# Kernel optimization log

Measured on AMD Instinct MI355X. Metric: run time of the kernel, lower is better.

The kernel has to match this reference:

```python
import jax, jax.numpy as jnp
import numpy as np


def _conv(x, w, b, stride):
    y = jax.lax.conv_general_dilated(x, w, (stride, stride), [(1, 1), (1, 1)],
                                     dimension_numbers=('NCHW', 'OIHW', 'NCHW'))
    return y + b[None, :, None, None]


def _prelu(x, a):
    return jnp.where(x >= 0, x, a[None, :, None, None] * x)


def _conv2_block(x, wa, ba, aa, wb, bb, ab):
    # conv2 = stride-2 conv + PReLU, then stride-1 conv + PReLU (RIFE-style)
    x = _prelu(_conv(x, wa, ba, 2), aa)
    return _prelu(_conv(x, wb, bb, 1), ab)


def _halve_flow(flow):
    # F.interpolate(scale_factor=0.5, bilinear, align_corners=False) on exact
    # half-downsampling == 2x2 average pooling; then * 0.5 rescales flow units.
    B, C, H, W = flow.shape
    return flow.reshape(B, C, H // 2, 2, W // 2, 2).mean(axis=(3, 5)) * 0.5


def _splat_one(inp, flow):
    # inp [C,H,W], flow [2,H,W]: bilinear forward-splat (scatter-add) summation
    C, H, W = inp.shape
    gx = jnp.arange(W, dtype=flow.dtype)
    gy = jnp.arange(H, dtype=flow.dtype)
    fx = flow[0] + gx[None, :]  # target x coord per source pixel
    fy = flow[1] + gy[:, None]
    x0 = jnp.floor(fx); y0 = jnp.floor(fy)
    x1 = x0 + 1.0;      y1 = y0 + 1.0
    src = inp.reshape(C, H * W)
    out = jnp.zeros((C, H * W), inp.dtype)
    corners = [(x0, y0, (x1 - fx) * (y1 - fy)),
               (x1, y0, (fx - x0) * (y1 - fy)),
               (x0, y1, (x1 - fx) * (fy - y0)),
               (x1, y1, (fx - x0) * (fy - y0))]
    for xi, yi, w in corners:
        valid = (xi >= 0) & (xi < W) & (yi >= 0) & (yi < H)
        idx = yi.astype(jnp.int32) * W + xi.astype(jnp.int32)
        idx = jnp.where(valid, idx, 0).reshape(-1)
        wv = jnp.where(valid, w, 0.0).reshape(-1)
        out = out.at[:, idx].add(src * wv[None, :])
    return out.reshape(C, H, W)


def _softsplat_avg(inp, flow):
    # strType='average': splat features and a ones channel, divide by count
    num = jax.vmap(_splat_one)(inp, flow)
    cnt = jax.vmap(_splat_one)(jnp.ones_like(inp[:, :1]), flow)
    return num / jnp.where(cnt == 0.0, 1.0, cnt)


def setup_inputs() -> dict:
    key = jax.random.key(0)
    ks = jax.random.split(key, 12)
    B, H, W = 16, 512, 512
    d = {
        'img': jax.random.normal(ks[0], (B, 3, H, W), jnp.float32),
        'flow': jax.random.normal(ks[1], (B, 2, H, W), jnp.float32) * 4.0,
    }
    c = 16
    chans = [(3, c), (c, 2 * c), (2 * c, 4 * c), (4 * c, 8 * c)]
    for i, (ci, co) in enumerate(chans, start=1):
        ka, kb = jax.random.split(ks[1 + i], 2)
        d[f'w{i}a'] = jax.random.normal(ka, (co, ci, 3, 3), jnp.float32) * 0.1
        d[f'b{i}a'] = jnp.zeros((co,), jnp.float32)
        d[f'a{i}a'] = jnp.full((co,), 0.25, jnp.float32)
        d[f'w{i}b'] = jax.random.normal(kb, (co, co, 3, 3), jnp.float32) * 0.1
        d[f'b{i}b'] = jnp.zeros((co,), jnp.float32)
        d[f'a{i}b'] = jnp.full((co,), 0.25, jnp.float32)
    return d


def reference(img, flow,
              w1a, b1a, a1a, w1b, b1b, a1b,
              w2a, b2a, a2a, w2b, b2b, a2b,
              w3a, b3a, a3a, w3b, b3b, a3b,
              w4a, b4a, a4a, w4b, b4b, a4b):
    blocks = [(w1a, b1a, a1a, w1b, b1b, a1b),
              (w2a, b2a, a2a, w2b, b2b, a2b),
              (w3a, b3a, a3a, w3b, b3b, a3b),
              (w4a, b4a, a4a, w4b, b4b, a4b)]
    feat = img
    fl = flow
    pyr = []
    for blk in blocks:
        feat = _conv2_block(feat, *blk)
        fl = _halve_flow(fl)
        pyr.append(_softsplat_avg(feat, fl))
    return tuple(pyr)
```

## Files before the change

kernel.cpp:

```cpp
#include <hip/hip_runtime.h>

#define CDIV(a, b) (((a) + (b) - 1) / (b))

typedef float __attribute__((ext_vector_type(2))) f32x2;
typedef float __attribute__((ext_vector_type(4))) f32x4;

__device__ __forceinline__ void pk_fma(f32x2& d, f32x2 a, f32x2 b) {
    asm("v_pk_fma_f32 %0, %1, %2, %0" : "+v"(d) : "v"(a), "v"(b));
}

__device__ __forceinline__ void fadd_native(float* p, float v) {
    unsafeAtomicAdd(p, v);
}

template <int STRIDE, int TW, int TH, int CB>
__global__ __launch_bounds__(256)
void conv3x3_pk_kernel(const float* __restrict__ in,
                       const float* __restrict__ wgt,
                       const float* __restrict__ bias,
                       const float* __restrict__ alpha,
                       float* __restrict__ out,
                       int Ci, int Hi, int Wi, int Co, int Ho, int Wo,
                       int nTX) {
    constexpr int KO  = 16;
    constexpr int PX  = TW / 16, PY = TH / 16;
    constexpr int ISX = TW * STRIDE + 2;
    constexpr int ISY = TH * STRIDE + 2;
    constexpr int ISS = ISX * ISY;
    constexpr int NST = (CB * ISS + 255) / 256;
    constexpr int NWT = (CB * 9 * KO + 255) / 256;
    __shared__ float s_in[CB * ISS];
    __shared__ __align__(16) float s_wt[CB * 9 * KO];

    const int b   = blockIdx.z;
    const int co0 = blockIdx.y * KO;
    const int tX  = (blockIdx.x % nTX) * TW;
    const int tY  = (blockIdx.x / nTX) * TH;
    const int t   = threadIdx.x;
    const int tcx = t & 15, tcy = t >> 4;
    const int ox0 = PX * tcx, oy0 = PY * tcy;
    const int HiWi = Hi * Wi;

    int  poff[NST];
    bool pval[NST];
    const int ix0 = tX * STRIDE - 1, iy0 = tY * STRIDE - 1;
#pragma unroll
    for (int s = 0; s < NST; ++s) {
        const int i = t + s * 256;
        int off = 0; bool v = false;
        if (i < CB * ISS) {
            const int p = i / ISS, j = i - p * ISS;
            const int r = j / ISX, c = j - r * ISX;
            const int gy = iy0 + r, gx = ix0 + c;
            v = (gy >= 0) && (gy < Hi) && (gx >= 0) && (gx < Wi);
            off = v ? (p * HiWi + gy * Wi + gx) : 0;
        }
        poff[s] = off; pval[s] = v;
    }
    int  wofs[NWT], wdst[NWT];
    bool wvs[NWT];
#pragma unroll
    for (int s = 0; s < NWT; ++s) {
        const int j = t + s * 256;
        bool v = j < CB * 9 * KO;
        int ofs = 0, dst = 0;
        if (v) {
            const int p = j / (9 * KO), rem = j - p * 9 * KO;
            const int k = rem / KO, ko = rem - k * KO;
            ofs = ((co0 + ko) * Ci + p) * 9 + k;
            dst = (p * 9 + k) * KO + ko;
        }
        wofs[s] = ofs; wdst[s] = dst; wvs[s] = v;
    }

    f32x2 acc2[KO / 2][PY][PX];
#pragma unroll
    for (int cp = 0; cp < KO / 2; ++cp)
#pragma unroll
        for (int dy = 0; dy < PY; ++dy)
#pragma unroll
            for (int dx = 0; dx < PX; ++dx) acc2[cp][dy][dx] = (f32x2){0.f, 0.f};

    const float* inb = in + (size_t)b * Ci * HiWi;

    float rs[NST], rw[NWT];
#pragma unroll
    for (int s = 0; s < NST; ++s) rs[s] = pval[s] ? inb[poff[s]] : 0.f;
#pragma unroll
    for (int s = 0; s < NWT; ++s) rw[s] = wvs[s] ? wgt[wofs[s]] : 0.f;

    const int bx = ox0 * STRIDE, by = oy0 * STRIDE;

    for (int ci = 0; ci < Ci; ci += CB) {
        __syncthreads();
#pragma unroll
        for (int s = 0; s < NST; ++s) {
            const int i = t + s * 256;
            if (i < CB * ISS) s_in[i] = rs[s];
        }
#pragma unroll
        for (int s = 0; s < NWT; ++s)
            if (wvs[s]) s_wt[wdst[s]] = rw[s];
        if (ci + CB < Ci) {
            const float* nb = inb + (size_t)(ci + CB) * HiWi;
            const int w9 = (ci + CB) * 9;
#pragma unroll
            for (int s = 0; s < NST; ++s) rs[s] = pval[s] ? nb[poff[s]] : 0.f;
#pragma unroll
            for (int s = 0; s < NWT; ++s)
                rw[s] = wvs[s] ? wgt[wofs[s] + w9] : 0.f;
        }
        __syncthreads();

#pragma unroll
        for (int p = 0; p < CB; ++p) {
            const float* sp = s_in + p * ISS;
#pragma unroll
            for (int ky = 0; ky < 3; ++ky)
#pragma unroll
                for (int kx = 0; kx < 3; ++kx) {
                    const int k = ky * 3 + kx;
                    f32x2 t2[PY][PX];
#pragma unroll
                    for (int dy = 0; dy < PY; ++dy)
#pragma unroll
                        for (int dx = 0; dx < PX; ++dx) {
                            const float tv =
                                sp[(by + dy * STRIDE + ky) * ISX + bx +
                                   dx * STRIDE + kx];
                            t2[dy][dx] = (f32x2){tv, tv};
                        }
                    const float* wb = s_wt + (p * 9 + k) * KO;
#pragma unroll
                    for (int kq = 0; kq < KO / 4; ++kq) {
                        const f32x4 w4 =
                            *reinterpret_cast<const f32x4*>(wb + 4 * kq);
                        const f32x2 wlo = {w4[0], w4[1]};
                        const f32x2 whi = {w4[2], w4[3]};
#pragma unroll
                        for (int dy = 0; dy < PY; ++dy)
#pragma unroll
                            for (int dx = 0; dx < PX; ++dx) {
                                pk_fma(acc2[2 * kq][dy][dx], t2[dy][dx], wlo);
                                pk_fma(acc2[2 * kq + 1][dy][dx], t2[dy][dx], whi);
                            }
                    }
                }
        }
    }

#pragma unroll
    for (int cp = 0; cp < KO / 2; ++cp)
#pragma unroll
        for (int h = 0; h < 2; ++h) {
            const int co = co0 + 2 * cp + h;
            const float bv = bias[co], av = alpha[co];
#pragma unroll
            for (int dy = 0; dy < PY; ++dy) {
                const int oy = tY + oy0 + dy;
#pragma unroll
                for (int dx = 0; dx < PX; ++dx) {
                    const int ox = tX + ox0 + dx;
                    float v = acc2[cp][dy][dx][h] + bv;
                    v = v >= 0.f ? v : av * v;
                    out[(((size_t)b * Co + co) * Ho + oy) * Wo + ox] = v;
                }
            }
        }
}

__global__ void halve_flow_kernel(const float* __restrict__ in,
                                  float* __restrict__ out,
                                  int BC, int Ho, int Wo, int Hi, int Wi) {
    const int idx = blockIdx.x * blockDim.x + threadIdx.x;
    const int total = BC * Ho * Wo;
    if (idx >= total) return;
    const int wo = idx % Wo;
    int t = idx / Wo;
    const int ho = t % Ho;
    const int bc = t / Ho;
    const float* p = in + ((size_t)bc * Hi + 2 * ho) * Wi + 2 * wo;
    out[idx] = (p[0] + p[1] + p[Wi] + p[Wi + 1]) * 0.125f;
}

__global__ void splat_outlier_kernel(const float* __restrict__ feat,
                                     const float* __restrict__ flow,
                                     float* __restrict__ num,
                                     float* __restrict__ cnt,
                                     int B, int C, int H, int W, float thr) {
    const int HW = H * W;
    const int idx = blockIdx.x * blockDim.x + threadIdx.x;
    if (idx >= B * HW) return;
    const int b = idx / HW, px = idx - b * HW;
    const int y = px / W, x = px - y * W;
    const float dx = flow[(size_t)b * 2 * HW + px];
    const float dy = flow[(size_t)b * 2 * HW + HW + px];
    if (fabsf(dx) <= thr && fabsf(dy) <= thr) return;
    const float fx = dx + (float)x, fy = dy + (float)y;
    const float x0f = floorf(fx), y0f = floorf(fy);
    const int x0 = (int)x0f, y0 = (int)y0f;
    const float ax = fx - x0f, ay = fy - y0f;
    const float w[4] = {(1.f - ax) * (1.f - ay), ax * (1.f - ay),
                        (1.f - ax) * ay,         ax * ay};
    const int cx[4] = {x0, x0 + 1, x0, x0 + 1};
    const int cy[4] = {y0, y0, y0 + 1, y0 + 1};
    float* cb = cnt + (size_t)b * HW;
    for (int k = 0; k < 4; ++k) {
        if (cx[k] < 0 || cx[k] >= W || cy[k] < 0 || cy[k] >= H) continue;
        if (w[k] == 0.f) continue;
        const size_t d = (size_t)cy[k] * W + cx[k];
        fadd_native(cb + d, w[k]);
        for (int c = 0; c < C; ++c)
            fadd_native(num + ((size_t)b * C + c) * HW + d,
                        feat[((size_t)b * C + c) * HW + px] * w[k]);
    }
}

template <int TS, int K, int NCH, int HCAP>
__global__ __launch_bounds__(256)
void splat_gather2_kernel(const float* __restrict__ feat,
                          const float* __restrict__ flow,
                          const float* __restrict__ cnt_ov,
                          float* __restrict__ out,
                          int C, int H, int W, int nTX) {
    constexpr int WS   = TS + 2 * K;
    constexpr int SSTR = WS + 1;
    constexpr int RUN  = TS * TS / 256;
    constexpr int TPR  = TS / RUN;
    constexpr int NSF  = (WS * WS + 255) / 256;
    constexpr float THR = (float)(K - 1);
    __shared__ __align__(8) float s_xy[2 * WS * SSTR];
    __shared__ float s_feat[WS * SSTR];
    __shared__ unsigned short s_hit[256 * HCAP];

    const int b   = blockIdx.z;
    const int c0  = blockIdx.y * NCH;
    const int tx0 = (blockIdx.x % nTX) * TS;
    const int ty0 = (blockIdx.x / nTX) * TS;
    const int t   = threadIdx.x;
    const int HW  = H * W;
    const float* flx = flow + (size_t)b * 2 * HW;
    const float* fly = flx + HW;
    const float* fb  = feat + ((size_t)b * C + c0) * HW;

    int  foff[NSF], sdst[NSF];
    bool fval[NSF];
#pragma unroll
    for (int s = 0; s < NSF; ++s) {
        const int i = t + s * 256;
        foff[s] = 0; sdst[s] = 0; fval[s] = false;
        if (i < WS * WS) {
            const int wsy = i / WS, wsx = i - wsy * WS;
            const int gy = ty0 - K + wsy, gx = tx0 - K + wsx;
            const int off = wsy * SSTR + wsx;
            sdst[s] = off;
            float fxr = 1e9f, fyr = 1e9f;
            if (gy >= 0 && gy < H && gx >= 0 && gx < W) {
                fval[s] = true;
                foff[s] = gy * W + gx;
                const float dxf = flx[foff[s]];
                const float dyf = fly[foff[s]];
                if (fabsf(dxf) <= THR && fabsf(dyf) <= THR) {
                    fxr = dxf + (float)(gx - tx0);
                    fyr = dyf + (float)(gy - ty0);
                }
            }
            *reinterpret_cast<f32x2*>(&s_xy[2 * off]) = (f32x2){fxr, fyr};
        }
    }
    __syncthreads();

    const int r  = t / TPR;
    const int x0 = (t % TPR) * RUN;

    int n = 0;
    unsigned short* hl = s_hit + t * HCAP;
#pragma unroll
    for (int dy = 0; dy <= 2 * K; ++dy) {
        const int wsy = r + dy;
        const int base = wsy * SSTR + x0;
#pragma unroll
        for (int dxx = 0; dxx < RUN + 2 * K; ++dxx) {
            const f32x2 xy =
                *reinterpret_cast<const f32x2*>(&s_xy[2 * (base + dxx)]);
            const float ty = xy[1] - (float)r;
            const float ux = xy[0] - (float)x0;
            if (ty > -1.f && ty < 1.f && ux > -1.f && ux < (float)RUN &&
                n < HCAP) {
                hl[n] = (unsigned short)((wsy << 6) | (x0 + dxx));
                ++n;
            }
        }
    }

    const int gyd = ty0 + r;
    const size_t rowoff = (size_t)gyd * W + (tx0 + x0);
    float cv_ov[RUN];
#pragma unroll
    for (int m = 0; m < RUN; ++m)
        cv_ov[m] = cnt_ov[(size_t)b * HW + rowoff + m];

    float rs[NSF];
#pragma unroll
    for (int s = 0; s < NSF; ++s) rs[s] = fval[s] ? fb[foff[s]] : 0.f;

    float inv[RUN];
#pragma unroll
    for (int ch = 0; ch < NCH; ++ch) {
        __syncthreads();
#pragma unroll
        for (int s = 0; s < NSF; ++s)
            if (t + s * 256 < WS * WS) s_feat[sdst[s]] = rs[s];
        if (ch + 1 < NCH) {
            const float* nfb = fb + (size_t)(ch + 1) * HW;
#pragma unroll
            for (int s = 0; s < NSF; ++s) rs[s] = fval[s] ? nfb[foff[s]] : 0.f;
        }
        __syncthreads();

        float a[RUN];
        float cw[RUN];
#pragma unroll
        for (int m = 0; m < RUN; ++m) { a[m] = 0.f; cw[m] = 0.f; }
        for (int k = 0; k < n; ++k) {
            const int idx = hl[k];
            const int off = (idx >> 6) * SSTR + (idx & 63);
            const f32x2 xy = *reinterpret_cast<const f32x2*>(&s_xy[2 * off]);
            const float f = s_feat[off];
            const float wy = 1.f - fabsf(xy[1] - (float)r);
            const float ux = xy[0] - (float)x0;
#pragma unroll
            for (int m = 0; m < RUN; ++m) {
                const float wm = fmaxf(0.f, 1.f - fabsf(ux - (float)m)) * wy;
                a[m] = fmaf(wm, f, a[m]);
                if (ch == 0) cw[m] += wm;
            }
        }
        if (ch == 0) {
#pragma unroll
            for (int m = 0; m < RUN; ++m) {
                const float cv = cw[m] + cv_ov[m];
                inv[m] = 1.f / ((cv == 0.f) ? 1.f : cv);
            }
        }

        const size_t go = ((size_t)b * C + (c0 + ch)) * HW + rowoff;
        if constexpr (RUN == 4) {
            float vv[4];
#pragma unroll
            for (int m = 0; m < 4; ++m) {
                float x = a[m];
                if (cv_ov[m] != 0.f) x += out[go + m];
                vv[m] = x * inv[m];
            }
            float4 v4 = {vv[0], vv[1], vv[2], vv[3]};
            *reinterpret_cast<float4*>(out + go) = v4;
        } else {
            float x = a[0];
            if (cv_ov[0] != 0.f) x += out[go];
            out[go] = x * inv[0];
        }
    }
}

extern "C" void kernel_launch(void* const* d_in, const int* in_sizes, int n_in,
                              void* d_out, int out_size, void* d_ws, size_t ws_size,
                              hipStream_t stream) {
    (void)in_sizes; (void)n_in; (void)ws_size;

    const float* img  = (const float*)d_in[0];
    const float* flow = (const float*)d_in[1];
    const float* P[4][6];
    for (int i = 0; i < 4; ++i)
        for (int j = 0; j < 6; ++j)
            P[i][j] = (const float*)d_in[2 + 6 * i + j];

    const int Bn = 16;
    float* ws = (float*)d_ws;
    float* bufA = ws;
    float* bufB = ws + 16777216;
    float* flA  = ws + 33554432;
    float* flB  = ws + 35651584;
    float* cnt  = ws + 36175872;
    float* out  = (float*)d_out;

    hipMemsetAsync(d_out, 0, (size_t)out_size * sizeof(float), stream);

    auto halve = [&](const float* in, float* o, int Hi, int Wi) {
        const int Ho = Hi / 2, Wo = Wi / 2;
        const int total = Bn * 2 * Ho * Wo;
        hipLaunchKernelGGL(halve_flow_kernel, dim3(CDIV(total, 256)), dim3(256),
                           0, stream, in, o, Bn * 2, Ho, Wo, Hi, Wi);
    };

    float* p1 = out;
    float* p2 = p1 + (size_t)Bn * 16 * 256 * 256;
    float* p3 = p2 + (size_t)Bn * 32 * 128 * 128;
    float* p4 = p3 + (size_t)Bn * 64 * 64 * 64;

#define CONV(S, TWv, THv, CBv, inp, wi, o, Ci_, Hi_, Wi_, Co_)                 \
    do {                                                                       \
        const int Ho_ = (Hi_) / (S), Wo_ = (Wi_) / (S);                        \
        const int nTX_ = Wo_ / (TWv), nTY_ = Ho_ / (THv);                      \
        hipLaunchKernelGGL((conv3x3_pk_kernel<S, TWv, THv, CBv>),              \
                           dim3(nTX_ * nTY_, (Co_) / 16, Bn), dim3(256), 0,    \
                           stream, inp, P[wi][0 + 3 * ((S) == 1)],             \
                           P[wi][1 + 3 * ((S) == 1)], P[wi][2 + 3 * ((S) == 1)],\
                           o, Ci_, Hi_, Wi_, Co_, Ho_, Wo_, nTX_);             \
    } while (0)

#define SPLAT(TSv, Kv, NCHv, HCAPv, featp, flp, op, C_, H_, W_, thr)           \
    do {                                                                       \
        hipMemsetAsync(cnt, 0, (size_t)Bn * (H_) * (W_) * sizeof(float),       \
                       stream);                                                \
        hipLaunchKernelGGL(splat_outlier_kernel,                               \
                           dim3(CDIV(Bn * (H_) * (W_), 256)), dim3(256), 0,    \
                           stream, featp, flp, op, cnt, Bn, C_, H_, W_, thr);  \
        hipLaunchKernelGGL((splat_gather2_kernel<TSv, Kv, NCHv, HCAPv>),       \
                           dim3(((W_) / (TSv)) * ((H_) / (TSv)),               \
                                (C_) / (NCHv), Bn),                            \
                           dim3(256), 0, stream, featp, flp, cnt, op,          \
                           C_, H_, W_, (W_) / (TSv));                          \
    } while (0)

    CONV(2, 32, 32, 1, img,  0, bufA, 3, 512, 512, 16);
    CONV(1, 32, 32, 2, bufA, 0, bufB, 16, 256, 256, 16);
    halve(flow, flA, 512, 512);
    SPLAT(32, 4, 16, 32, bufB, flA, p1, 16, 256, 256, 3.f);

    CONV(2, 32, 32, 1, bufB, 1, bufA, 16, 256, 256, 32);
    CONV(1, 32, 32, 2, bufA, 1, bufB, 32, 128, 128, 32);
    halve(flA, flB, 256, 256);
    SPLAT(32, 3, 16, 32, bufB, flB, p2, 32, 128, 128, 2.f);

    CONV(2, 32, 16, 1, bufB, 2, bufA, 32, 128, 128, 64);
    CONV(1, 32, 16, 2, bufA, 2, bufB, 64, 64, 64, 64);
    halve(flB, flA, 128, 128);
    SPLAT(16, 2, 16, 16, bufB, flA, p3, 64, 64, 64, 1.f);

    CONV(2, 16, 16, 1, bufB, 3, bufA, 64, 64, 64, 128);
    CONV(1, 16, 16, 2, bufA, 3, bufB, 128, 32, 32, 128);
    halve(flA, flB, 64, 64);
    SPLAT(16, 2, 16, 16, bufB, flB, p4, 128, 32, 32, 1.f);

#undef CONV
#undef SPLAT
}
```

Before: 1.023 ms.

## Split conv input channels across blocks with partial-sum reduction and transposed weights

Rewrites the 3x3 conv kernel to read pre-transposed weights straight from global memory (a new transpose kernel runs before each conv) instead of staging them in shared memory. Deeper layers split the input-channel loop across extra blocks, write partial sums into the output buffer as scratch, and fuse the reduction with bias and PReLU in a separate pass. The level-1 splat is deferred to the end so the output region can serve as scratch, and tile shapes are retuned. This aims to raise occupancy on the small, low-parallelism late layers, at the cost of extra partial-sum traffic and more kernel launches.

After: 1.129 ms. 10.3% more time.

```diff
diff --git a/kernel.cpp b/kernel.cpp
--- a/kernel.cpp
+++ b/kernel.cpp
@@ -13,160 +13,168 @@
     unsafeAtomicAdd(p, v);
 }
 
-template <int STRIDE, int TW, int TH, int CB>
+__global__ void wtrans_kernel(const float* __restrict__ w,
+                              float* __restrict__ wT, int Co, int Ci) {
+    const int idx = blockIdx.x * blockDim.x + threadIdx.x;
+    if (idx >= Co * Ci * 9) return;
+    const int co = idx / (Ci * 9);
+    const int rem = idx - co * Ci * 9;
+    const int ci = rem / 9, k = rem - ci * 9;
+    wT[((size_t)ci * 9 + k) * Co + co] = w[idx];
+}
+
+template <int STRIDE, int TW, int TH, int PART>
 __global__ __launch_bounds__(256)
-void conv3x3_pk_kernel(const float* __restrict__ in,
-                       const float* __restrict__ wgt,
-                       const float* __restrict__ bias,
-                       const float* __restrict__ alpha,
-                       float* __restrict__ out,
-                       int Ci, int Hi, int Wi, int Co, int Ho, int Wo,
-                       int nTX) {
-    constexpr int KO  = 16;
-    constexpr int PX  = TW / 16, PY = TH / 16;
-    constexpr int ISX = TW * STRIDE + 2;
-    constexpr int ISY = TH * STRIDE + 2;
-    constexpr int ISS = ISX * ISY;
-    constexpr int NST = (CB * ISS + 255) / 256;
-    constexpr int NWT = (CB * 9 * KO + 255) / 256;
-    __shared__ float s_in[CB * ISS];
-    __shared__ __align__(16) float s_wt[CB * 9 * KO];
+void conv3x3_v3(const float* __restrict__ in, const float* __restrict__ wT,
+                const float* __restrict__ bias, const float* __restrict__ alpha,
+                float* __restrict__ out, int Ci, int CL, int Hi, int Wi,
+                int Co, int Ho, int Wo, int nTX, int nCog) {
+    constexpr int PX = TW / 16, PY = TH / 16;
+    constexpr int ISX = TW * STRIDE + 2, ISY = TH * STRIDE + 2;
+    constexpr int PAD = ISX + 1;
+    constexpr int NEL = ISY * ISX;
+    constexpr int NST = (NEL + 255) / 256;
+    __shared__ float s_in[ISY * PAD];
 
     const int b   = blockIdx.z;
-    const int co0 = blockIdx.y * KO;
+    const int cog = blockIdx.y % nCog;
+    const int spl = blockIdx.y / nCog;
+    const int co0 = cog * 16;
+    const int ci0 = spl * CL;
     const int tX  = (blockIdx.x % nTX) * TW;
     const int tY  = (blockIdx.x / nTX) * TH;
     const int t   = threadIdx.x;
     const int tcx = t & 15, tcy = t >> 4;
-    const int ox0 = PX * tcx, oy0 = PY * tcy;
     const int HiWi = Hi * Wi;
 
-    int  poff[NST];
+    int poff[NST], pdst[NST];
     bool pval[NST];
     const int ix0 = tX * STRIDE - 1, iy0 = tY * STRIDE - 1;
 #pragma unroll
     for (int s = 0; s < NST; ++s) {
         const int i = t + s * 256;
-        int off = 0; bool v = false;
-        if (i < CB * ISS) {
-            const int p = i / ISS, j = i - p * ISS;
-            const int r = j / ISX, c = j - r * ISX;
+        poff[s] = 0; pdst[s] = 0; pval[s] = false;
+        if (i < NEL) {
+            const int r = i / ISX, c = i - r * ISX;
             const int gy = iy0 + r, gx = ix0 + c;
-            v = (gy >= 0) && (gy < Hi) && (gx >= 0) && (gx < Wi);
-            off = v ? (p * HiWi + gy * Wi + gx) : 0;
-        }
-        poff[s] = off; pval[s] = v;
-    }
-    int  wofs[NWT], wdst[NWT];
-    bool wvs[NWT];
-#pragma unroll
-    for (int s = 0; s < NWT; ++s) {
-        const int j = t + s * 256;
-        bool v = j < CB * 9 * KO;
-        int ofs = 0, dst = 0;
-        if (v) {
-            const int p = j / (9 * KO), rem = j - p * 9 * KO;
-            const int k = rem / KO, ko = rem - k * KO;
-            ofs = ((co0 + ko) * Ci + p) * 9 + k;
-            dst = (p * 9 + k) * KO + ko;
-        }
-        wofs[s] = ofs; wdst[s] = dst; wvs[s] = v;
-    }
-
-    f32x2 acc2[KO / 2][PY][PX];
-#pragma unroll
-    for (int cp = 0; cp < KO / 2; ++cp)
-#pragma unroll
-        for (int dy = 0; dy < PY; ++dy)
-#pragma unroll
-            for (int dx = 0; dx < PX; ++dx) acc2[cp][dy][dx] = (f32x2){0.f, 0.f};
-
-    const float* inb = in + (size_t)b * Ci * HiWi;
-
-    float rs[NST], rw[NWT];
+            pval[s] = (gy >= 0) && (gy < Hi) && (gx >= 0) && (gx < Wi);
+            poff[s] = pval[s] ? gy * Wi + gx : 0;
+            pdst[s] = r * PAD + c;
+        }
+    }
+
+    f32x2 acc[8][PY][PX];
+#pragma unroll
+    for (int p = 0; p < 8; ++p)
+#pragma unroll
+        for (int py = 0; py < PY; ++py)
+#pragma unroll
+            for (int m = 0; m < PX; ++m) acc[p][py][m] = (f32x2){0.f, 0.f};
+
+    const float* inb = in + ((size_t)b * Ci + ci0) * HiWi;
+    float rs[NST];
 #pragma unroll
     for (int s = 0; s < NST; ++s) rs[s] = pval[s] ? inb[poff[s]] : 0.f;
-#pragma unroll
-    for (int s = 0; s < NWT; ++s) rw[s] = wvs[s] ? wgt[wofs[s]] : 0.f;
-
-    const int bx = ox0 * STRIDE, by = oy0 * STRIDE;
-
-    for (int ci = 0; ci < Ci; ci += CB) {
+
+    for (int cc = 0; cc < CL; ++cc) {
         __syncthreads();
 #pragma unroll
-        for (int s = 0; s < NST; ++s) {
-            const int i = t + s * 256;
-            if (i < CB * ISS) s_in[i] = rs[s];
-        }
-#pragma unroll
-        for (int s = 0; s < NWT; ++s)
-            if (wvs[s]) s_wt[wdst[s]] = rw[s];
-        if (ci + CB < Ci) {
-            const float* nb = inb + (size_t)(ci + CB) * HiWi;
-            const int w9 = (ci + CB) * 9;
+        for (int s = 0; s < NST; ++s)
+            if (t + s * 256 < NEL) s_in[pdst[s]] = rs[s];
+        if (cc + 1 < CL) {
+            const float* nb = inb + (size_t)(cc + 1) * HiWi;
 #pragma unroll
             for (int s = 0; s < NST; ++s) rs[s] = pval[s] ? nb[poff[s]] : 0.f;
-#pragma unroll
-            for (int s = 0; s < NWT; ++s)
-                rw[s] = wvs[s] ? wgt[wofs[s] + w9] : 0.f;
         }
         __syncthreads();
 
-#pragma unroll
-        for (int p = 0; p < CB; ++p) {
-            const float* sp = s_in + p * ISS;
-#pragma unroll
-            for (int ky = 0; ky < 3; ++ky)
-#pragma unroll
-                for (int kx = 0; kx < 3; ++kx) {
-                    const int k = ky * 3 + kx;
-                    f32x2 t2[PY][PX];
-#pragma unroll
-                    for (int dy = 0; dy < PY; ++dy)
-#pragma unroll
-                        for (int dx = 0; dx < PX; ++dx) {
-                            const float tv =
-                                sp[(by + dy * STRIDE + ky) * ISX + bx +
-                                   dx * STRIDE + kx];
-                            t2[dy][dx] = (f32x2){tv, tv};
+        const float* wrow = wT + (size_t)(ci0 + cc) * 9 * Co + co0;
+#pragma unroll
+        for (int ky = 0; ky < 3; ++ky)
+#pragma unroll
+            for (int kx = 0; kx < 3; ++kx) {
+                f32x2 t2[PY][PX];
+#pragma unroll
+                for (int py = 0; py < PY; ++py)
+#pragma unroll
+                    for (int m = 0; m < PX; ++m) {
+                        const float tv =
+                            s_in[((tcy + 16 * py) * STRIDE + ky) * PAD +
+                                 (tcx + 16 * m) * STRIDE + kx];
+                        t2[py][m] = (f32x2){tv, tv};
+                    }
+                const float* wk = wrow + (ky * 3 + kx) * Co;
+#pragma unroll
+                for (int kq = 0; kq < 4; ++kq) {
+                    const f32x4 w4 =
+                        *reinterpret_cast<const f32x4*>(wk + 4 * kq);
+                    const f32x2 wlo = {w4[0], w4[1]};
+                    const f32x2 whi = {w4[2], w4[3]};
+#pragma unroll
+                    for (int py = 0; py < PY; ++py)
+#pragma unroll
+                        for (int m = 0; m < PX; ++m) {
+                            pk_fma(acc[2 * kq][py][m], t2[py][m], wlo);
+                            pk_fma(acc[2 * kq + 1][py][m], t2[py][m], whi);
                         }
-                    const float* wb = s_wt + (p * 9 + k) * KO;
-#pragma unroll
-                    for (int kq = 0; kq < KO / 4; ++kq) {
-                        const f32x4 w4 =
-                            *reinterpret_cast<const f32x4*>(wb + 4 * kq);
-                        const f32x2 wlo = {w4[0], w4[1]};
-                        const f32x2 whi = {w4[2], w4[3]};
-#pragma unroll
-                        for (int dy = 0; dy < PY; ++dy)
-#pragma unroll
-                            for (int dx = 0; dx < PX; ++dx) {
-                                pk_fma(acc2[2 * kq][dy][dx], t2[dy][dx], wlo);
-                                pk_fma(acc2[2 * kq + 1][dy][dx], t2[dy][dx], whi);
-                            }
+                }
+            }
+    }
+
+    const size_t HoWo = (size_t)Ho * Wo;
+#pragma unroll
+    for (int p = 0; p < 8; ++p) {
+        const int cbase = co0 + 4 * (p >> 1) + 2 * (p & 1);
+#pragma unroll
+        for (int h = 0; h < 2; ++h) {
+            const int co = cbase + h;
+            float bv = 0.f, av = 0.f;
+            if constexpr (!PART) { bv = bias[co]; av = alpha[co]; }
+#pragma unroll
+            for (int py = 0; py < PY; ++py) {
+                const int oy = tY + tcy + 16 * py;
+#pragma unroll
+                for (int m = 0; m < PX; ++m) {
+                    const int ox = tX + tcx + 16 * m;
+                    float v = acc[p][py][m][h];
+                    if constexpr (PART) {
+                        out[((size_t)((spl << 4) + b) * Co + co) * HoWo +
+                            (size_t)oy * Wo + ox] = v;
+                    } else {
+                        v += bv;
+                        v = v >= 0.f ? v : av * v;
+                        out[((size_t)b * Co + co) * HoWo +
+                            (size_t)oy * Wo + ox] = v;
                     }
                 }
-        }
-    }
-
-#pragma unroll
-    for (int cp = 0; cp < KO / 2; ++cp)
-#pragma unroll
-        for (int h = 0; h < 2; ++h) {
-            const int co = co0 + 2 * cp + h;
-            const float bv = bias[co], av = alpha[co];
-#pragma unroll
-            for (int dy = 0; dy < PY; ++dy) {
-                const int oy = tY + oy0 + dy;
-#pragma unroll
-                for (int dx = 0; dx < PX; ++dx) {
-                    const int ox = tX + ox0 + dx;
-                    float v = acc2[cp][dy][dx][h] + bv;
-                    v = v >= 0.f ? v : av * v;
-                    out[(((size_t)b * Co + co) * Ho + oy) * Wo + ox] = v;
-                }
-            }
-        }
+            }
+        }
+    }
+}
+
+__global__ void reduce_prelu_kernel(const float* __restrict__ part,
+                                    const float* __restrict__ bias,
+                                    const float* __restrict__ alpha,
+                                    float* __restrict__ out,
+                                    int nspl, int N4, int Co, int HW) {
+    const int i4 = blockIdx.x * blockDim.x + threadIdx.x;
+    if (i4 >= N4) return;
+    const size_t idx = (size_t)i4 * 4;
+    const size_t N = (size_t)N4 * 4;
+    f32x4 s = *reinterpret_cast<const f32x4*>(part + idx);
+    for (int sp = 1; sp < nspl; ++sp) {
+        const f32x4 q =
+            *reinterpret_cast<const f32x4*>(part + (size_t)sp * N + idx);
+        s[0] += q[0]; s[1] += q[1]; s[2] += q[2]; s[3] += q[3];
+    }
+    const int co = (int)((idx / HW) % Co);
+    const float bv = bias[co], av = alpha[co];
+    float4 o;
+    float v0 = s[0] + bv; o.x = v0 >= 0.f ? v0 : av * v0;
+    float v1 = s[1] + bv; o.y = v1 >= 0.f ? v1 : av * v1;
+    float v2 = s[2] + bv; o.z = v2 >= 0.f ? v2 : av * v2;
+    float v3 = s[3] + bv; o.w = v3 >= 0.f ? v3 : av * v3;
+    *reinterpret_cast<float4*>(out + idx) = o;
 }
 
 __global__ void halve_flow_kernel(const float* __restrict__ in,
@@ -376,13 +384,22 @@
             P[i][j] = (const float*)d_in[2 + 6 * i + j];
 
     const int Bn = 16;
-    float* ws = (float*)d_ws;
-    float* bufA = ws;
-    float* bufB = ws + 16777216;
-    float* flA  = ws + 33554432;
-    float* flB  = ws + 35651584;
-    float* cnt  = ws + 36175872;
-    float* out  = (float*)d_out;
+    float* ws  = (float*)d_ws;
+    float* W0  = ws;
+    float* A   = ws + 16777216;
+    float* Bf  = ws + 25165824;
+    float* fl1 = ws + 33554432;
+    float* fl2 = ws + 35651584;
+    float* fl3 = ws + 36175872;
+    float* fl4 = ws + 36306944;
+    float* cnt = ws + 36339712;
+    float* wTb = ws + 37388288;
+    float* out = (float*)d_out;
+
+    float* p1 = out;
+    float* p2 = p1 + (size_t)Bn * 16 * 256 * 256;
+    float* p3 = p2 + (size_t)Bn * 32 * 128 * 128;
+    float* p4 = p3 + (size_t)Bn * 64 * 64 * 64;
 
     hipMemsetAsync(d_out, 0, (size_t)out_size * sizeof(float), stream);
 
@@ -393,20 +410,30 @@
                            0, stream, in, o, Bn * 2, Ho, Wo, Hi, Wi);
     };
 
-    float* p1 = out;
-    float* p2 = p1 + (size_t)Bn * 16 * 256 * 256;
-    float* p3 = p2 + (size_t)Bn * 32 * 128 * 128;
-    float* p4 = p3 + (size_t)Bn * 64 * 64 * 64;
-
-#define CONV(S, TWv, THv, CBv, inp, wi, o, Ci_, Hi_, Wi_, Co_)                 \
+#define DO_CONV(S, TWv, THv, CSPLv, inp, Wp, Bp, Ap, dst, Ci_, Hi_, Wi_, Co_)  \
     do {                                                                       \
         const int Ho_ = (Hi_) / (S), Wo_ = (Wi_) / (S);                        \
         const int nTX_ = Wo_ / (TWv), nTY_ = Ho_ / (THv);                      \
-        hipLaunchKernelGGL((conv3x3_pk_kernel<S, TWv, THv, CBv>),              \
-                           dim3(nTX_ * nTY_, (Co_) / 16, Bn), dim3(256), 0,    \
-                           stream, inp, P[wi][0 + 3 * ((S) == 1)],             \
-                           P[wi][1 + 3 * ((S) == 1)], P[wi][2 + 3 * ((S) == 1)],\
-                           o, Ci_, Hi_, Wi_, Co_, Ho_, Wo_, nTX_);             \
+        const int nCog_ = (Co_) / 16;                                          \
+        hipLaunchKernelGGL(wtrans_kernel, dim3(CDIV((Co_) * (Ci_) * 9, 256)),  \
+                           dim3(256), 0, stream, Wp, wTb, Co_, Ci_);           \
+        if ((CSPLv) == 1) {                                                    \
+            hipLaunchKernelGGL((conv3x3_v3<S, TWv, THv, 0>),                   \
+                               dim3(nTX_ * nTY_, nCog_, Bn), dim3(256), 0,     \
+                               stream, inp, wTb, Bp, Ap, dst, Ci_, Ci_,        \
+                               Hi_, Wi_, Co_, Ho_, Wo_, nTX_, nCog_);          \
+        } else {                                                               \
+            hipLaunchKernelGGL((conv3x3_v3<S, TWv, THv, 1>),                   \
+                               dim3(nTX_ * nTY_, nCog_ * (CSPLv), Bn),         \
+                               dim3(256), 0, stream, inp, wTb,                 \
+                               (const float*)nullptr, (const float*)nullptr,   \
+                               p1, Ci_, (Ci_) / (CSPLv), Hi_, Wi_, Co_,        \
+                               Ho_, Wo_, nTX_, nCog_);                         \
+            const int N4_ = Bn * (Co_) * Ho_ * Wo_ / 4;                        \
+            hipLaunchKernelGGL(reduce_prelu_kernel, dim3(CDIV(N4_, 256)),      \
+                               dim3(256), 0, stream, p1, Bp, Ap, dst, CSPLv,   \
+                               N4_, Co_, Ho_ * Wo_);                           \
+        }                                                                      \
     } while (0)
 
 #define SPLAT(TSv, Kv, NCHv, HCAPv, featp, flp, op, C_, H_, W_, thr)           \
@@ -423,26 +450,28 @@
                            C_, H_, W_, (W_) / (TSv));                          \
     } while (0)
 
-    CONV(2, 32, 32, 1, img,  0, bufA, 3, 512, 512, 16);
-    CONV(1, 32, 32, 2, bufA, 0, bufB, 16, 256, 256, 16);
-    halve(flow, flA, 512, 512);
-    SPLAT(32, 4, 16, 32, bufB, flA, p1, 16, 256, 256, 3.f);
-
-    CONV(2, 32, 32, 1, bufB, 1, bufA, 16, 256, 256, 32);
-    CONV(1, 32, 32, 2, bufA, 1, bufB, 32, 128, 128, 32);
-    halve(flA, flB, 256, 256);
-    SPLAT(32, 3, 16, 32, bufB, flB, p2, 32, 128, 128, 2.f);
-
-    CONV(2, 32, 16, 1, bufB, 2, bufA, 32, 128, 128, 64);
-    CONV(1, 32, 16, 2, bufA, 2, bufB, 64, 64, 64, 64);
-    halve(flB, flA, 128, 128);
-    SPLAT(16, 2, 16, 16, bufB, flA, p3, 64, 64, 64, 1.f);
-
-    CONV(2, 16, 16, 1, bufB, 3, bufA, 64, 64, 64, 128);
-    CONV(1, 16, 16, 2, bufA, 3, bufB, 128, 32, 32, 128);
-    halve(flA, flB, 64, 64);
-    SPLAT(16, 2, 16, 16, bufB, flB, p4, 128, 32, 32, 1.f);
-
-#undef CONV
+    DO_CONV(2, 32, 16, 1, img, P[0][0], P[0][1], P[0][2], p1, 3, 512, 512, 16);
+    DO_CONV(1, 32, 32, 1, p1,  P[0][3], P[0][4], P[0][5], W0, 16, 256, 256, 16);
+    halve(flow, fl1, 512, 512);
+
+    DO_CONV(2, 32, 16, 1, W0, P[1][0], P[1][1], P[1][2], A,  16, 256, 256, 32);
+    DO_CONV(1, 32, 32, 2, A,  P[1][3], P[1][4], P[1][5], Bf, 32, 128, 128, 32);
+    halve(fl1, fl2, 256, 256);
+    SPLAT(32, 3, 16, 32, Bf, fl2, p2, 32, 128, 128, 2.f);
+
+    DO_CONV(2, 32, 16, 2, Bf, P[2][0], P[2][1], P[2][2], A,  32, 128, 128, 64);
+    DO_CONV(1, 32, 32, 4, A,  P[2][3], P[2][4], P[2][5], Bf, 64, 64, 64, 64);
+    halve(fl2, fl3, 128, 128);
+    SPLAT(16, 2, 16, 16, Bf, fl3, p3, 64, 64, 64, 1.f);
+
+    DO_CONV(2, 32, 16, 4, Bf, P[3][0], P[3][1], P[3][2], A,  64, 64, 64, 128);
+    DO_CONV(1, 32, 32, 8, A,  P[3][3], P[3][4], P[3][5], Bf, 128, 32, 32, 128);
+    halve(fl3, fl4, 64, 64);
+    SPLAT(16, 2, 16, 16, Bf, fl4, p4, 128, 32, 32, 1.f);
+
+    hipMemsetAsync(p1, 0, (size_t)16777216 * sizeof(float), stream);
+    SPLAT(32, 4, 16, 32, W0, fl1, p1, 16, 256, 256, 3.f);
+
+#undef DO_CONV
 #undef SPLAT
 }
```
